# Kernel optimization log

Hardware: AMD Instinct MI355X
Metric: run time of the kernel (lower is better)

Reference implementation:

```python
import jax, jax.numpy as jnp
import numpy as np

N_FACTS = 512
D = 256          # object_dim == query_dim
HG = 256         # g hidden / output width
HF1, HF2 = 256, 512
OUT_F = 159


def setup_inputs() -> dict:
    key = jax.random.key(0)
    ks = jax.random.split(key, 16)
    s = 0.02
    return {
        "x": jax.random.normal(ks[0], (N_FACTS, D), dtype=jnp.float32),
        "q": jax.random.normal(ks[1], (D,), dtype=jnp.float32),
        # MLP g: input 3*D -> 256 -> 256 -> 256, ReLU after every layer (nonlinear=True)
        "g_W1": jax.random.normal(ks[2], (3 * D, HG), dtype=jnp.float32) * s,
        "g_b1": jnp.zeros((HG,), dtype=jnp.float32),
        "g_W2": jax.random.normal(ks[3], (HG, HG), dtype=jnp.float32) * s,
        "g_b2": jnp.zeros((HG,), dtype=jnp.float32),
        "g_W3": jax.random.normal(ks[4], (HG, HG), dtype=jnp.float32) * s,
        "g_b3": jnp.zeros((HG,), dtype=jnp.float32),
        # MLP f: 256 -> 256 -> 512 -> 159, ReLU on hidden layers only
        "f_W1": jax.random.normal(ks[5], (HG, HF1), dtype=jnp.float32) * s,
        "f_b1": jnp.zeros((HF1,), dtype=jnp.float32),
        "f_W2": jax.random.normal(ks[6], (HF1, HF2), dtype=jnp.float32) * s,
        "f_b2": jnp.zeros((HF2,), dtype=jnp.float32),
        "f_W3": jax.random.normal(ks[7], (HF2, OUT_F), dtype=jnp.float32) * s,
        "f_b3": jnp.zeros((OUT_F,), dtype=jnp.float32),
    }


def reference(x, q, g_W1, g_b1, g_W2, g_b2, g_W3, g_b3,
              f_W1, f_b1, f_W2, f_b2, f_W3, f_b3):
    # Original builds pair_concat[k] = cat(x[i], x[j], q) for k = j*n + i.
    # Decompose g's first linear over the concat blocks to avoid materializing
    # the (n^2, 3D) tensor: same math, three small matmuls + broadcast add.
    d = x.shape[1]
    a = x @ g_W1[:d]            # (n, HG), contribution of xi
    b = x @ g_W1[d:2 * d]       # (n, HG), contribution of xj
    c = q @ g_W1[2 * d:]        # (HG,),  contribution of q
    # pair (j, i): xj varies along axis 0, xi along axis 1
    h = jax.nn.relu(b[:, None, :] + a[None, :, :] + c + g_b1)   # (n, n, HG)
    h = jax.nn.relu(h @ g_W2 + g_b2)
    rel = jax.nn.relu(h @ g_W3 + g_b3)                          # (n, n, HG)
    emb = rel.sum(axis=(0, 1))[None, :]                         # (1, HG) = sum over all pairs
    y = jax.nn.relu(emb @ f_W1 + f_b1)
    y = jax.nn.relu(y @ f_W2 + f_b2)
    out = y @ f_W3 + f_b3                                       # (1, OUT_F)
    return out
```

## Files before the change

kernel.cpp:

```cpp
#include <hip/hip_runtime.h>
#include <hip/hip_bf16.h>

typedef __attribute__((ext_vector_type(4))) float  f32x4;
typedef __attribute__((ext_vector_type(8))) __bf16 bf16x8;

static __device__ __forceinline__ unsigned short bfbits(float x) {
    return __builtin_bit_cast(unsigned short, (__bf16)x);
}

__global__ __launch_bounds__(256) void prep_all(
    const float* __restrict__ x, const float* __restrict__ q,
    const float* __restrict__ gW1, const float* __restrict__ gb1,
    const float* __restrict__ gW2, const float* __restrict__ gW3,
    float* __restrict__ a, float* __restrict__ b,
    float* __restrict__ cc, float* __restrict__ emb,
    unsigned short* __restrict__ w2t, unsigned short* __restrict__ w3t)
{
    const int t = threadIdx.x;
    const int bid = blockIdx.x;
    if (bid < 128) {
        __shared__ float xs[4][256];
        const int r0 = bid * 4;
        #pragma unroll
        for (int r = 0; r < 4; ++r) xs[r][t] = x[(r0 + r) * 256 + t];
        __syncthreads();
        float aa[4] = {0.f, 0.f, 0.f, 0.f}, bb[4] = {0.f, 0.f, 0.f, 0.f};
        #pragma unroll 4
        for (int d = 0; d < 256; ++d) {
            const float wa = gW1[d * 256 + t];
            const float wb = gW1[(256 + d) * 256 + t];
            #pragma unroll
            for (int r = 0; r < 4; ++r) {
                aa[r] = fmaf(xs[r][d], wa, aa[r]);
                bb[r] = fmaf(xs[r][d], wb, bb[r]);
            }
        }
        #pragma unroll
        for (int r = 0; r < 4; ++r) {
            a[(r0 + r) * 256 + t] = aa[r];
            b[(r0 + r) * 256 + t] = bb[r];
        }
    } else if (bid == 128) {
        float acc = gb1[t];
        #pragma unroll 8
        for (int d = 0; d < 256; ++d) acc = fmaf(q[d], gW1[(512 + d) * 256 + t], acc);
        cc[t] = acc;
        emb[t] = 0.f;
    } else {
        __shared__ unsigned short tile[64][65];
        const int bb_ = bid - 129;
        const float* src = (bb_ < 16) ? gW2 : gW3;
        unsigned short* dst = (bb_ < 16) ? w2t : w3t;
        const int bidx = bb_ & 15;
        const int br = (bidx >> 2) * 64;
        const int bc = (bidx & 3) * 64;
        const int tr = t >> 6;
        const int tc = t & 63;
        #pragma unroll
        for (int rr = 0; rr < 16; ++rr) {
            const int r = tr * 16 + rr;
            tile[r][tc] = bfbits(src[(br + r) * 256 + bc + tc]);
        }
        __syncthreads();
        #pragma unroll
        for (int rr = 0; rr < 16; ++rr) {
            const int r = tr * 16 + rr;
            dst[(bc + r) * 256 + br + tc] = tile[tc][r];
        }
    }
}

__global__ __launch_bounds__(512, 2) void rn_main(
    const float* __restrict__ ga, const float* __restrict__ gb,
    const float* __restrict__ cc,
    const unsigned short* __restrict__ w2t, const unsigned short* __restrict__ w3t,
    const float* __restrict__ gb2, const float* __restrict__ gb3,
    float* __restrict__ emb)
{
    __shared__ __bf16 h1[64 * 256];
    __shared__ __bf16 h2[64 * 256];

    const int t = threadIdx.x;
    const int j = blockIdx.x;
    const int lane = t & 63;
    const int wave = t >> 6;
    const int l16 = lane & 15;
    const int lk = lane >> 4;
    const int wcol = wave * 32;

    const int k0 = (t & 31) << 3;
    f32x4 bc0, bc1;
    {
        const f32x4 g0 = *reinterpret_cast<const f32x4*>(gb + j * 256 + k0);
        const f32x4 g1 = *reinterpret_cast<const f32x4*>(gb + j * 256 + k0 + 4);
        const f32x4 c0 = *reinterpret_cast<const f32x4*>(cc + k0);
        const f32x4 c1 = *reinterpret_cast<const f32x4*>(cc + k0 + 4);
        #pragma unroll
        for (int e = 0; e < 4; ++e) { bc0[e] = g0[e] + c0[e]; bc1[e] = g1[e] + c1[e]; }
    }

    bf16x8 B2[2][8], B3[2][8];
    float bias2[2], bias3[2];
    #pragma unroll
    for (int ns = 0; ns < 2; ++ns) {
        const int col = wcol + ns * 16 + l16;
        bias2[ns] = gb2[col];
        bias3[ns] = gb3[col];
        #pragma unroll
        for (int ks = 0; ks < 8; ++ks) {
            const int koff = ks * 32 + lk * 8;
            B2[ns][ks] = *reinterpret_cast<const bf16x8*>(w2t + col * 256 + koff);
            B3[ns][ks] = *reinterpret_cast<const bf16x8*>(w3t + col * 256 + koff);
        }
    }
    float colsum[2] = {0.f, 0.f};

    #define GEN_H1(I0)                                                              \
    {                                                                               \
        _Pragma("unroll")                                                           \
        for (int r = 0; r < 4; ++r) {                                               \
            const int m = (t >> 5) + r * 16;                                        \
            const f32x4 a0 = *reinterpret_cast<const f32x4*>(ga + ((I0) + m) * 256 + k0);     \
            const f32x4 a1 = *reinterpret_cast<const f32x4*>(ga + ((I0) + m) * 256 + k0 + 4); \
            bf16x8 pk;                                                              \
            _Pragma("unroll")                                                       \
            for (int e = 0; e < 4; ++e) {                                           \
                pk[e]     = (__bf16)fmaxf(a0[e] + bc0[e], 0.f);                     \
                pk[e + 4] = (__bf16)fmaxf(a1[e] + bc1[e], 0.f);                     \
            }                                                                       \
            *reinterpret_cast<bf16x8*>(&h1[(m * 256 + k0) ^ ((m & 7) << 3)]) = pk;  \
        }                                                                           \
    }

    GEN_H1(0);
    __syncthreads();

    for (int it = 0; it < 8; ++it) {
        #pragma unroll
        for (int ms = 0; ms < 4; ++ms) {
            const int row = ms * 16 + l16;
            bf16x8 A[8];
            #pragma unroll
            for (int ks = 0; ks < 8; ++ks) {
                const int koff = ks * 32 + lk * 8;
                A[ks] = *reinterpret_cast<const bf16x8*>(&h1[(row * 256 + koff) ^ ((row & 7) << 3)]);
            }
            #pragma unroll
            for (int ns = 0; ns < 2; ++ns) {
                f32x4 acc = {0.f, 0.f, 0.f, 0.f};
                #pragma unroll
                for (int ks = 0; ks < 8; ++ks)
                    acc = __builtin_amdgcn_mfma_f32_16x16x32_bf16(A[ks], B2[ns][ks], acc, 0, 0, 0);
                const int ccol = wcol + ns * 16 + l16;
                #pragma unroll
                for (int reg = 0; reg < 4; ++reg) {
                    const float v = fmaxf(acc[reg] + bias2[ns], 0.f);
                    const int rr = ms * 16 + lk * 4 + reg;
                    h2[(rr * 256 + ccol) ^ ((rr & 7) << 3)] = (__bf16)v;
                }
            }
        }
        __syncthreads();

        if (it < 7) GEN_H1((it + 1) * 64);
        #pragma unroll
        for (int ms = 0; ms < 4; ++ms) {
            const int row = ms * 16 + l16;
            bf16x8 A[8];
            #pragma unroll
            for (int ks = 0; ks < 8; ++ks) {
                const int koff = ks * 32 + lk * 8;
                A[ks] = *reinterpret_cast<const bf16x8*>(&h2[(row * 256 + koff) ^ ((row & 7) << 3)]);
            }
            #pragma unroll
            for (int ns = 0; ns < 2; ++ns) {
                f32x4 acc = {0.f, 0.f, 0.f, 0.f};
                #pragma unroll
                for (int ks = 0; ks < 8; ++ks)
                    acc = __builtin_amdgcn_mfma_f32_16x16x32_bf16(A[ks], B3[ns][ks], acc, 0, 0, 0);
                float s = 0.f;
                #pragma unroll
                for (int reg = 0; reg < 4; ++reg)
                    s += fmaxf(acc[reg] + bias3[ns], 0.f);
                colsum[ns] += s;
            }
        }
        __syncthreads();
    }

    #pragma unroll
    for (int ns = 0; ns < 2; ++ns) {
        float v = colsum[ns];
        v += __shfl_xor(v, 16, 64);
        v += __shfl_xor(v, 32, 64);
        if (lane < 16) atomicAdd(&emb[wcol + ns * 16 + l16], v);
    }
    #undef GEN_H1
}

__global__ __launch_bounds__(1024) void rn_final(
    const float* __restrict__ emb,
    const float* __restrict__ fW1, const float* __restrict__ fb1,
    const float* __restrict__ fW2, const float* __restrict__ fb2,
    const float* __restrict__ fW3, const float* __restrict__ fb3,
    float* __restrict__ out)
{
    __shared__ float e_s[256];
    __shared__ float red[1024];
    __shared__ float y1[256];
    __shared__ float y2[512];
    const int t = threadIdx.x;
    if (t < 256) e_s[t] = emb[t];
    __syncthreads();
    {
        const int col = t & 255, ks = t >> 8;
        float acc = 0.f;
        #pragma unroll 8
        for (int k = ks * 64; k < ks * 64 + 64; ++k) acc = fmaf(e_s[k], fW1[k * 256 + col], acc);
        red[ks * 256 + col] = acc;
    }
    __syncthreads();
    if (t < 256)
        y1[t] = fmaxf(red[t] + red[256 + t] + red[512 + t] + red[768 + t] + fb1[t], 0.f);
    __syncthreads();
    {
        const int col = t & 511, ks = t >> 9;
        float acc = 0.f;
        #pragma unroll 8
        for (int k = ks * 128; k < ks * 128 + 128; ++k) acc = fmaf(y1[k], fW2[k * 512 + col], acc);
        red[ks * 512 + col] = acc;
    }
    __syncthreads();
    if (t < 512) y2[t] = fmaxf(red[t] + red[512 + t] + fb2[t], 0.f);
    __syncthreads();
    {
        const int col = t & 255, ks = t >> 8;
        if (col < 159) {
            float acc = 0.f;
            #pragma unroll 8
            for (int k = ks * 128; k < ks * 128 + 128; ++k) acc = fmaf(y2[k], fW3[k * 159 + col], acc);
            red[ks * 256 + col] = acc;
        }
    }
    __syncthreads();
    if (t < 159)
        out[t] = red[t] + red[256 + t] + red[512 + t] + red[768 + t] + fb3[t];
}

extern "C" void kernel_launch(void* const* d_in, const int* in_sizes, int n_in,
                              void* d_out, int out_size, void* d_ws, size_t ws_size,
                              hipStream_t stream)
{
    const float* x   = (const float*)d_in[0];
    const float* q   = (const float*)d_in[1];
    const float* gW1 = (const float*)d_in[2];
    const float* gb1 = (const float*)d_in[3];
    const float* gW2 = (const float*)d_in[4];
    const float* gb2 = (const float*)d_in[5];
    const float* gW3 = (const float*)d_in[6];
    const float* gb3 = (const float*)d_in[7];
    const float* fW1 = (const float*)d_in[8];
    const float* fb1 = (const float*)d_in[9];
    const float* fW2 = (const float*)d_in[10];
    const float* fb2 = (const float*)d_in[11];
    const float* fW3 = (const float*)d_in[12];
    const float* fb3 = (const float*)d_in[13];
    float* out = (float*)d_out;

    char* ws = (char*)d_ws;
    float* a_  = (float*)(ws);
    float* b_  = (float*)(ws + 512 * 1024);
    float* cc  = (float*)(ws + 1024 * 1024);
    float* emb = (float*)(ws + 1024 * 1024 + 1024);
    unsigned short* w2t = (unsigned short*)(ws + 1024 * 1024 + 2048);
    unsigned short* w3t = (unsigned short*)(ws + 1024 * 1024 + 2048 + 128 * 1024);

    prep_all<<<161, 256, 0, stream>>>(x, q, gW1, gb1, gW2, gW3, a_, b_, cc, emb, w2t, w3t);
    rn_main<<<512, 512, 0, stream>>>(a_, b_, cc, w2t, w3t, gb2, gb3, emb);
    rn_final<<<1, 1024, 0, stream>>>(emb, fW1, fb1, fW2, fb2, fW3, fb3, out);
}
```

Measured before the change: 219.2 us.

## Fuse final MLP into main kernel via last-block ticket and prefetch next h1 tile

Removes the separate rn_final launch. The last rn_main block to finish, detected with an atomic ticket counter, now runs the f-MLP. Inside the main loop, the global loads for the next h1 tile are issued before the layer-2 MFMAs, and their conversion to bf16 is deferred until after layer 3, to hide load latency. prep_all is split into twice as many blocks with 2 rows each, for more parallelism in the a/b projection. This adds shared memory and register pressure (prefetched f32x4 buffers) and relies on threadfence/atomic ordering for correctness.

```diff
diff --git a/kernel.cpp b/kernel.cpp
--- a/kernel.cpp
+++ b/kernel.cpp
@@ -14,41 +14,43 @@
     const float* __restrict__ gW2, const float* __restrict__ gW3,
     float* __restrict__ a, float* __restrict__ b,
     float* __restrict__ cc, float* __restrict__ emb,
+    unsigned int* __restrict__ ticket,
     unsigned short* __restrict__ w2t, unsigned short* __restrict__ w3t)
 {
     const int t = threadIdx.x;
     const int bid = blockIdx.x;
-    if (bid < 128) {
-        __shared__ float xs[4][256];
-        const int r0 = bid * 4;
-        #pragma unroll
-        for (int r = 0; r < 4; ++r) xs[r][t] = x[(r0 + r) * 256 + t];
+    if (bid < 256) {
+        __shared__ float xs[2][256];
+        const int r0 = bid * 2;
+        #pragma unroll
+        for (int r = 0; r < 2; ++r) xs[r][t] = x[(r0 + r) * 256 + t];
         __syncthreads();
-        float aa[4] = {0.f, 0.f, 0.f, 0.f}, bb[4] = {0.f, 0.f, 0.f, 0.f};
+        float aa[2] = {0.f, 0.f}, bb[2] = {0.f, 0.f};
         #pragma unroll 4
         for (int d = 0; d < 256; ++d) {
             const float wa = gW1[d * 256 + t];
             const float wb = gW1[(256 + d) * 256 + t];
             #pragma unroll
-            for (int r = 0; r < 4; ++r) {
+            for (int r = 0; r < 2; ++r) {
                 aa[r] = fmaf(xs[r][d], wa, aa[r]);
                 bb[r] = fmaf(xs[r][d], wb, bb[r]);
             }
         }
         #pragma unroll
-        for (int r = 0; r < 4; ++r) {
+        for (int r = 0; r < 2; ++r) {
             a[(r0 + r) * 256 + t] = aa[r];
             b[(r0 + r) * 256 + t] = bb[r];
         }
-    } else if (bid == 128) {
+    } else if (bid == 256) {
         float acc = gb1[t];
         #pragma unroll 8
         for (int d = 0; d < 256; ++d) acc = fmaf(q[d], gW1[(512 + d) * 256 + t], acc);
         cc[t] = acc;
         emb[t] = 0.f;
+        if (t == 0) *ticket = 0u;
     } else {
         __shared__ unsigned short tile[64][65];
-        const int bb_ = bid - 129;
+        const int bb_ = bid - 257;
         const float* src = (bb_ < 16) ? gW2 : gW3;
         unsigned short* dst = (bb_ < 16) ? w2t : w3t;
         const int bidx = bb_ & 15;
@@ -75,10 +77,16 @@
     const float* __restrict__ cc,
     const unsigned short* __restrict__ w2t, const unsigned short* __restrict__ w3t,
     const float* __restrict__ gb2, const float* __restrict__ gb3,
-    float* __restrict__ emb)
+    float* __restrict__ emb, unsigned int* __restrict__ ticket,
+    const float* __restrict__ fW1, const float* __restrict__ fb1,
+    const float* __restrict__ fW2, const float* __restrict__ fb2,
+    const float* __restrict__ fW3, const float* __restrict__ fb3,
+    float* __restrict__ out)
 {
     __shared__ __bf16 h1[64 * 256];
     __shared__ __bf16 h2[64 * 256];
+    __shared__ float fe[256], fy1[256], fy2[512], fred[512];
+    __shared__ int is_last_s;
 
     const int t = threadIdx.x;
     const int j = blockIdx.x;
@@ -115,27 +123,34 @@
     }
     float colsum[2] = {0.f, 0.f};
 
-    #define GEN_H1(I0)                                                              \
-    {                                                                               \
-        _Pragma("unroll")                                                           \
-        for (int r = 0; r < 4; ++r) {                                               \
-            const int m = (t >> 5) + r * 16;                                        \
-            const f32x4 a0 = *reinterpret_cast<const f32x4*>(ga + ((I0) + m) * 256 + k0);     \
-            const f32x4 a1 = *reinterpret_cast<const f32x4*>(ga + ((I0) + m) * 256 + k0 + 4); \
-            bf16x8 pk;                                                              \
-            _Pragma("unroll")                                                       \
-            for (int e = 0; e < 4; ++e) {                                           \
-                pk[e]     = (__bf16)fmaxf(a0[e] + bc0[e], 0.f);                     \
-                pk[e + 4] = (__bf16)fmaxf(a1[e] + bc1[e], 0.f);                     \
-            }                                                                       \
-            *reinterpret_cast<bf16x8*>(&h1[(m * 256 + k0) ^ ((m & 7) << 3)]) = pk;  \
-        }                                                                           \
-    }
-
-    GEN_H1(0);
+    #pragma unroll
+    for (int r = 0; r < 4; ++r) {
+        const int m = (t >> 5) + r * 16;
+        const f32x4 a0 = *reinterpret_cast<const f32x4*>(ga + m * 256 + k0);
+        const f32x4 a1 = *reinterpret_cast<const f32x4*>(ga + m * 256 + k0 + 4);
+        bf16x8 pk;
+        #pragma unroll
+        for (int e = 0; e < 4; ++e) {
+            pk[e]     = (__bf16)fmaxf(a0[e] + bc0[e], 0.f);
+            pk[e + 4] = (__bf16)fmaxf(a1[e] + bc1[e], 0.f);
+        }
+        *reinterpret_cast<bf16x8*>(&h1[(m * 256 + k0) ^ ((m & 7) << 3)]) = pk;
+    }
     __syncthreads();
 
     for (int it = 0; it < 8; ++it) {
+        f32x4 g0[4], g1[4];
+        if (it < 7) {
+            #pragma unroll
+            for (int r = 0; r < 4; ++r) {
+                const int m = (t >> 5) + r * 16;
+                const float* p = ga + ((it + 1) * 64 + m) * 256 + k0;
+                g0[r] = *reinterpret_cast<const f32x4*>(p);
+                g1[r] = *reinterpret_cast<const f32x4*>(p + 4);
+            }
+        }
+        __builtin_amdgcn_sched_barrier(0);
+
         #pragma unroll
         for (int ms = 0; ms < 4; ++ms) {
             const int row = ms * 16 + l16;
@@ -162,7 +177,6 @@
         }
         __syncthreads();
 
-        if (it < 7) GEN_H1((it + 1) * 64);
         #pragma unroll
         for (int ms = 0; ms < 4; ++ms) {
             const int row = ms * 16 + l16;
@@ -183,6 +197,19 @@
                 for (int reg = 0; reg < 4; ++reg)
                     s += fmaxf(acc[reg] + bias3[ns], 0.f);
                 colsum[ns] += s;
+            }
+        }
+        if (it < 7) {
+            #pragma unroll
+            for (int r = 0; r < 4; ++r) {
+                const int m = (t >> 5) + r * 16;
+                bf16x8 pk;
+                #pragma unroll
+                for (int e = 0; e < 4; ++e) {
+                    pk[e]     = (__bf16)fmaxf(g0[r][e] + bc0[e], 0.f);
+                    pk[e + 4] = (__bf16)fmaxf(g1[r][e] + bc1[e], 0.f);
+                }
+                *reinterpret_cast<bf16x8*>(&h1[(m * 256 + k0) ^ ((m & 7) << 3)]) = pk;
             }
         }
         __syncthreads();
@@ -195,56 +222,47 @@
         v += __shfl_xor(v, 32, 64);
         if (lane < 16) atomicAdd(&emb[wcol + ns * 16 + l16], v);
     }
-    #undef GEN_H1
-}
-
-__global__ __launch_bounds__(1024) void rn_final(
-    const float* __restrict__ emb,
-    const float* __restrict__ fW1, const float* __restrict__ fb1,
-    const float* __restrict__ fW2, const float* __restrict__ fb2,
-    const float* __restrict__ fW3, const float* __restrict__ fb3,
-    float* __restrict__ out)
-{
-    __shared__ float e_s[256];
-    __shared__ float red[1024];
-    __shared__ float y1[256];
-    __shared__ float y2[512];
-    const int t = threadIdx.x;
-    if (t < 256) e_s[t] = emb[t];
+
+    __syncthreads();
+    if (t == 0) {
+        __threadfence();
+        const unsigned int done = atomicAdd(ticket, 1u);
+        is_last_s = (done == 511u);
+    }
+    __syncthreads();
+    if (!is_last_s) return;
+
+    __threadfence();
+    if (t < 256) fe[t] = emb[t];
     __syncthreads();
     {
         const int col = t & 255, ks = t >> 8;
         float acc = 0.f;
         #pragma unroll 8
-        for (int k = ks * 64; k < ks * 64 + 64; ++k) acc = fmaf(e_s[k], fW1[k * 256 + col], acc);
-        red[ks * 256 + col] = acc;
-    }
-    __syncthreads();
-    if (t < 256)
-        y1[t] = fmaxf(red[t] + red[256 + t] + red[512 + t] + red[768 + t] + fb1[t], 0.f);
+        for (int k = ks * 128; k < ks * 128 + 128; ++k) acc = fmaf(fe[k], fW1[k * 256 + col], acc);
+        fred[ks * 256 + col] = acc;
+    }
+    __syncthreads();
+    if (t < 256) fy1[t] = fmaxf(fred[t] + fred[256 + t] + fb1[t], 0.f);
     __syncthreads();
     {
-        const int col = t & 511, ks = t >> 9;
-        float acc = 0.f;
+        float acc = fb2[t];
         #pragma unroll 8
-        for (int k = ks * 128; k < ks * 128 + 128; ++k) acc = fmaf(y1[k], fW2[k * 512 + col], acc);
-        red[ks * 512 + col] = acc;
-    }
-    __syncthreads();
-    if (t < 512) y2[t] = fmaxf(red[t] + red[512 + t] + fb2[t], 0.f);
+        for (int k = 0; k < 256; ++k) acc = fmaf(fy1[k], fW2[k * 512 + t], acc);
+        fy2[t] = fmaxf(acc, 0.f);
+    }
     __syncthreads();
     {
         const int col = t & 255, ks = t >> 8;
         if (col < 159) {
             float acc = 0.f;
             #pragma unroll 8
-            for (int k = ks * 128; k < ks * 128 + 128; ++k) acc = fmaf(y2[k], fW3[k * 159 + col], acc);
-            red[ks * 256 + col] = acc;
-        }
-    }
-    __syncthreads();
-    if (t < 159)
-        out[t] = red[t] + red[256 + t] + red[512 + t] + red[768 + t] + fb3[t];
+            for (int k = ks * 256; k < ks * 256 + 256; ++k) acc = fmaf(fy2[k], fW3[k * 159 + col], acc);
+            fred[ks * 256 + col] = acc;
+        }
+    }
+    __syncthreads();
+    if (t < 159) out[t] = fred[t] + fred[256 + t] + fb3[t];
 }
 
 extern "C" void kernel_launch(void* const* d_in, const int* in_sizes, int n_in,
@@ -272,10 +290,12 @@
     float* b_  = (float*)(ws + 512 * 1024);
     float* cc  = (float*)(ws + 1024 * 1024);
     float* emb = (float*)(ws + 1024 * 1024 + 1024);
-    unsigned short* w2t = (unsigned short*)(ws + 1024 * 1024 + 2048);
-    unsigned short* w3t = (unsigned short*)(ws + 1024 * 1024 + 2048 + 128 * 1024);
-
-    prep_all<<<161, 256, 0, stream>>>(x, q, gW1, gb1, gW2, gW3, a_, b_, cc, emb, w2t, w3t);
-    rn_main<<<512, 512, 0, stream>>>(a_, b_, cc, w2t, w3t, gb2, gb3, emb);
-    rn_final<<<1, 1024, 0, stream>>>(emb, fW1, fb1, fW2, fb2, fW3, fb3, out);
+    unsigned int* ticket = (unsigned int*)(ws + 1024 * 1024 + 2048);
+    unsigned short* w2t = (unsigned short*)(ws + 1024 * 1024 + 4096);
+    unsigned short* w3t = (unsigned short*)(ws + 1024 * 1024 + 4096 + 128 * 1024);
+
+    prep_all<<<289, 256, 0, stream>>>(x, q, gW1, gb1, gW2, gW3, a_, b_, cc, emb,
+                                      ticket, w2t, w3t);
+    rn_main<<<512, 512, 0, stream>>>(a_, b_, cc, w2t, w3t, gb2, gb3, emb, ticket,
+                                     fW1, fb1, fW2, fb2, fW3, fb3, out);
 }
```

Measured after the change: 275.7 us. 1.26x slower.
